# Kernel tuning notes

Measured on AMD Instinct MI355X. Metric: run time of the kernel, lower is better.

The kernel has to match this reference:

```python
import jax, jax.numpy as jnp
import numpy as np

TOPK_FRAC = 0.2

def _l2norm(v, eps=1e-12):
    return v / (jnp.linalg.norm(v) + eps)

def _spectral_normalize(w, u):
    # torch.nn.utils.spectral_norm forward: one power iteration (u,v detached),
    # sigma = u^T W v with gradient flowing through W only.
    wm = w.reshape(w.shape[0], -1)            # (out, in*kh*kw)
    v = _l2norm(jax.lax.stop_gradient(wm).T @ u)
    u_new = _l2norm(jax.lax.stop_gradient(wm) @ v)
    sigma = jnp.einsum('i,ij,j->', u_new, wm, v)
    return w / sigma

def setup_inputs() -> dict:
    key = jax.random.key(0)
    ks = jax.random.split(key, 5)
    N, C, H, W = 32, 512, 56, 56
    return {
        'x':  jax.random.normal(ks[0], (N, C, H, W), dtype=jnp.float32),
        'w1': jax.random.normal(ks[1], (C, C, 4, 4), dtype=jnp.float32) * 0.05,
        'w2': jax.random.normal(ks[2], (C, C, 1, 1), dtype=jnp.float32) * 0.05,
        'u1': jax.random.normal(ks[3], (C,), dtype=jnp.float32),
        'u2': jax.random.normal(ks[4], (C,), dtype=jnp.float32),
    }

def reference(x, w1, w2, u1, u2):
    N, C, H, W = x.shape
    # AdaptiveAvgPool2d(4): H,W divisible by 4 -> uniform 14x14 windows
    p = x.reshape(N, C, 4, H // 4, 4, W // 4).mean(axis=(3, 5))   # (N,C,4,4)
    p = jax.nn.sigmoid(p)
    # spectral-norm conv 4x4, valid, no bias -> fully reduces spatial to 1x1
    w1n = _spectral_normalize(w1, u1)                             # (C,C,4,4)
    h = jnp.einsum('ncij,ocij->no', p, w1n)                       # (N,C)
    h = jax.nn.relu(h)
    # spectral-norm conv 1x1
    w2n = _spectral_normalize(w2, u2).reshape(C, C)               # (out,in)
    s = jax.nn.sigmoid(jnp.einsum('nc,oc->no', h, w2n))           # (N,C)
    # sparse_ch: keep top int(0.2*C) channels per sample
    k = int(max(1, TOPK_FRAC * C))
    _, idx = jax.lax.top_k(s, k)                                  # (N,k)
    mask = jnp.zeros_like(s).at[jnp.arange(N)[:, None], idx].set(1.0)
    weight = (s * mask)[:, :, None, None]                         # (N,C,1,1)
    return x * weight
```

## Files before the change

kernel.cpp:

```cpp
#include <hip/hip_runtime.h>


#define KTOP 102

__device__ __forceinline__ float block_sum256(float v) {
  __shared__ float red[4];
  #pragma unroll
  for (int off = 32; off; off >>= 1) v += __shfl_down(v, off, 64);
  int lane = threadIdx.x & 63;
  int w = threadIdx.x >> 6;
  if (lane == 0) red[w] = v;
  __syncthreads();
  float r = 0.f;
  if (threadIdx.x == 0) r = red[0] + red[1] + red[2] + red[3];
  return r;
}

__global__ __launch_bounds__(256) void k_a(const float* __restrict__ x, const float* __restrict__ w1,
                                           const float* __restrict__ w2, const float* __restrict__ u1,
                                           const float* __restrict__ u2, float* __restrict__ p,
                                           float* __restrict__ part1, float* __restrict__ part1b,
                                           float* __restrict__ scal) {
  __shared__ float sx[3136];
  __shared__ float su[64];
  int b = blockIdx.x, t = threadIdx.x;
  if (b < 16384) {
    const float4* xp4 = (const float4*)(x + (size_t)b * 3136);
    float4* sx4 = (float4*)sx;
    for (int e = t; e < 784; e += 256) sx4[e] = xp4[e];
    __syncthreads();
    int w = t >> 4, lane = t & 15;
    int wr = w >> 2, wc = w & 3;
    float acc = 0.f;
    for (int e = lane; e < 196; e += 16) {
      int r = e / 14, cc = e - r * 14;
      acc += sx[(14 * wr + r) * 56 + 14 * wc + cc];
    }
    #pragma unroll
    for (int off = 8; off; off >>= 1) acc += __shfl_down(acc, off, 16);
    if (lane == 0) {
      float m = acc * (1.f / 196.f);
      p[(size_t)b * 16 + w] = 1.f / (1.f + expf(-m));
    }
  } else if (b < 16640) {
    int bb = b - 16384;
    if (bb == 0 && t < 4) scal[t] = 0.f;
    int jb = bb & 31, ic = bb >> 5;
    if (t < 64) su[t] = u1[ic * 64 + t];
    __syncthreads();
    int j = jb * 256 + t;
    const float* base = w1 + (size_t)(ic * 64) * 8192 + j;
    float acc = 0.f;
    #pragma unroll 4
    for (int i = 0; i < 64; ++i) acc += base[(size_t)i * 8192] * su[i];
    part1[ic * 8192 + j] = acc;
  } else {
    int bb = b - 16640;
    int jb = bb & 1, ic = bb >> 1;
    if (t < 64) su[t] = u2[ic * 64 + t];
    __syncthreads();
    int j = jb * 256 + t;
    const float* base = w2 + (size_t)(ic * 64) * 512 + j;
    float acc = 0.f;
    #pragma unroll 4
    for (int i = 0; i < 64; ++i) acc += base[(size_t)i * 512] * su[i];
    part1b[ic * 512 + j] = acc;
  }
}

__global__ __launch_bounds__(256) void k_b(const float* __restrict__ p, const float* __restrict__ w1,
                                           const float* __restrict__ part1, const float* __restrict__ part1b,
                                           float* __restrict__ part, float* __restrict__ t1,
                                           float* __restrict__ t1b, float* __restrict__ scal) {
  __shared__ float sp[32][132];
  __shared__ float sw[64][132];
  int b = blockIdx.x, t = threadIdx.x;
  if (b < 512) {
    int o0 = (b & 7) * 64;
    int k0 = (b >> 3) * 128;
    for (int idx = t; idx < 1024; idx += 256) {
      int r = idx >> 5, c4 = (idx & 31) << 2;
      *(float4*)&sp[r][c4] = *(const float4*)&p[(size_t)r * 8192 + k0 + c4];
    }
    for (int idx = t; idx < 2048; idx += 256) {
      int r = idx >> 5, c4 = (idx & 31) << 2;
      *(float4*)&sw[r][c4] = *(const float4*)&w1[(size_t)(o0 + r) * 8192 + k0 + c4];
    }
    __syncthreads();
    int m = t & 31, g = t >> 5;
    int n0 = g * 4;
    float acc[4][2] = {{0.f, 0.f}, {0.f, 0.f}, {0.f, 0.f}, {0.f, 0.f}};
    for (int kk = 0; kk < 128; kk += 4) {
      float4 wa = *(const float4*)&sw[m][kk];
      float4 wb = *(const float4*)&sw[m + 32][kk];
      #pragma unroll
      for (int ni = 0; ni < 4; ++ni) {
        float4 pv = *(const float4*)&sp[n0 + ni][kk];
        acc[ni][0] += pv.x * wa.x + pv.y * wa.y + pv.z * wa.z + pv.w * wa.w;
        acc[ni][1] += pv.x * wb.x + pv.y * wb.y + pv.z * wb.z + pv.w * wb.w;
      }
    }
    size_t base = (size_t)(b >> 3) * 16384;
    #pragma unroll
    for (int ni = 0; ni < 4; ++ni) {
      part[base + (n0 + ni) * 512 + o0 + m] = acc[ni][0];
      part[base + (n0 + ni) * 512 + o0 + m + 32] = acc[ni][1];
    }
  } else if (b < 544) {
    int j = (b - 512) * 256 + t;
    float s = 0.f;
    #pragma unroll
    for (int ic = 0; ic < 8; ++ic) s += part1[ic * 8192 + j];
    t1[j] = s;
    float tot = block_sum256(s * s);
    if (t == 0) atomicAdd(&scal[0], tot);
  } else {
    int j = (b - 544) * 256 + t;
    float s = 0.f;
    #pragma unroll
    for (int ic = 0; ic < 8; ++ic) s += part1b[ic * 512 + j];
    t1b[j] = s;
    float tot = block_sum256(s * s);
    if (t == 0) atomicAdd(&scal[1], tot);
  }
}

__global__ __launch_bounds__(256) void k_c(const float* __restrict__ part, const float* __restrict__ w1,
                                           const float* __restrict__ w2, const float* __restrict__ t1,
                                           const float* __restrict__ t1b, float* __restrict__ h,
                                           float* __restrict__ scal) {
  int b = blockIdx.x, t = threadIdx.x;
  if (b < 64) {
    int idx = b * 256 + t;
    float s = 0.f;
    for (int ks = 0; ks < 64; ++ks) s += part[(size_t)ks * 16384 + idx];
    h[idx] = fmaxf(s, 0.f);
  } else if (b < 576) {
    int i = b - 64;
    float inv = 1.f / (sqrtf(scal[0]) + 1e-12f);
    const float4* row = (const float4*)(w1 + (size_t)i * 8192);
    const float4* tv = (const float4*)t1;
    float acc = 0.f;
    for (int q = t; q < 2048; q += 256) {
      float4 a = row[q], v = tv[q];
      acc += a.x * v.x + a.y * v.y + a.z * v.z + a.w * v.w;
    }
    float tot = block_sum256(acc);
    if (t == 0) { float r = tot * inv; atomicAdd(&scal[2], r * r); }
  } else {
    int i = b - 576;
    float inv = 1.f / (sqrtf(scal[1]) + 1e-12f);
    const float4* row = (const float4*)(w2 + (size_t)i * 512);
    const float4* tv = (const float4*)t1b;
    float acc = 0.f;
    if (t < 128) {
      float4 a = row[t], v = tv[t];
      acc = a.x * v.x + a.y * v.y + a.z * v.z + a.w * v.w;
    }
    float tot = block_sum256(acc);
    if (t == 0) { float r = tot * inv; atomicAdd(&scal[3], r * r); }
  }
}

__global__ __launch_bounds__(256) void k_gemm2(const float* __restrict__ h, const float* __restrict__ w2,
                                               const float* __restrict__ scal, float* __restrict__ s_out) {
  int o = blockIdx.x, t = threadIdx.x;
  int w = t >> 6, lane = t & 63;
  float A2 = scal[2], B2 = scal[3];
  float sig1 = A2 / (sqrtf(A2) + 1e-12f);
  float sig2 = B2 / (sqrtf(B2) + 1e-12f);
  float inv = 1.f / (sig1 * sig2);
  const float4* wr = (const float4*)(w2 + (size_t)o * 512);
  float4 wa = wr[lane * 2], wb = wr[lane * 2 + 1];
  #pragma unroll
  for (int j = 0; j < 8; ++j) {
    int n = w * 8 + j;
    const float4* hr = (const float4*)(h + (size_t)n * 512);
    float4 ha = hr[lane * 2], hb = hr[lane * 2 + 1];
    float d = ha.x * wa.x + ha.y * wa.y + ha.z * wa.z + ha.w * wa.w
            + hb.x * wb.x + hb.y * wb.y + hb.z * wb.z + hb.w * wb.w;
    #pragma unroll
    for (int off = 32; off; off >>= 1) d += __shfl_down(d, off, 64);
    if (lane == 0) s_out[(size_t)n * 512 + o] = 1.f / (1.f + expf(-d * inv));
  }
}

__global__ __launch_bounds__(256) void k_topk(const float* __restrict__ s_in, float* __restrict__ wgt) {
  __shared__ float ss[512];
  __shared__ unsigned sb[512];
  __shared__ int cnt;
  int n = blockIdx.x, t = threadIdx.x;
  float v0 = s_in[(size_t)n * 512 + t];
  float v1 = s_in[(size_t)n * 512 + 256 + t];
  ss[t] = v0; ss[t + 256] = v1;
  sb[t] = __float_as_uint(v0); sb[t + 256] = __float_as_uint(v1);
  __syncthreads();
  int r = KTOP;
  unsigned prefix = 0u;
  for (int bit = 31; bit >= 0; --bit) {
    if (t == 0) cnt = 0;
    __syncthreads();
    unsigned hi = prefix | (1u << bit);
    unsigned mhi = ~((1u << bit) - 1u);
    unsigned long long c0 = __ballot((sb[t] & mhi) == hi);
    unsigned long long c1 = __ballot((sb[t + 256] & mhi) == hi);
    if ((t & 63) == 0) atomicAdd(&cnt, __popcll(c0) + __popcll(c1));
    __syncthreads();
    int c = cnt;
    __syncthreads();
    if (c >= r) prefix = hi; else r -= c;
  }
  if (t == 0) cnt = 0;
  __syncthreads();
  {
    unsigned long long g0 = __ballot(sb[t] > prefix);
    unsigned long long g1 = __ballot(sb[t + 256] > prefix);
    if ((t & 63) == 0) atomicAdd(&cnt, __popcll(g0) + __popcll(g1));
  }
  __syncthreads();
  int alloweq = KTOP - cnt;
  for (int e = t; e < 512; e += 256) {
    unsigned v = sb[e];
    bool keep = v > prefix;
    if (!keep && v == prefix) {
      int rank = 0;
      for (int j = 0; j < e; ++j) rank += (sb[j] == prefix);
      keep = rank < alloweq;
    }
    wgt[(size_t)n * 512 + e] = keep ? ss[e] : 0.f;
  }
}

__global__ __launch_bounds__(256) void k_scale(const float* __restrict__ x, const float* __restrict__ wgt,
                                               float* __restrict__ out) {
  int plane = blockIdx.x;
  float g = wgt[plane];
  const float4* xi = (const float4*)(x + (size_t)plane * 3136);
  float4* oo = (float4*)(out + (size_t)plane * 3136);
  for (int e = threadIdx.x; e < 784; e += 256) {
    float4 v = xi[e];
    v.x *= g; v.y *= g; v.z *= g; v.w *= g;
    oo[e] = v;
  }
}

extern "C" void kernel_launch(void* const* d_in, const int* in_sizes, int n_in,
                              void* d_out, int out_size, void* d_ws, size_t ws_size,
                              hipStream_t stream) {
  const float* x  = (const float*)d_in[0];
  const float* w1 = (const float*)d_in[1];
  const float* w2 = (const float*)d_in[2];
  const float* u1 = (const float*)d_in[3];
  const float* u2 = (const float*)d_in[4];
  float* out = (float*)d_out;
  float* ws = (float*)d_ws;

  float* scal   = ws + 0;
  float* t1     = ws + 4;
  float* t1b    = ws + 8196;
  float* p      = ws + 8708;
  float* part1  = ws + 270852;
  float* part1b = ws + 336388;
  float* part   = ws + 340484;
  float* h      = ws + 1389060;
  float* s      = ws + 1405444;
  float* wgt    = ws + 1421828;

  k_a<<<16656, 256, 0, stream>>>(x, w1, w2, u1, u2, p, part1, part1b, scal);
  k_b<<<546, 256, 0, stream>>>(p, w1, part1, part1b, part, t1, t1b, scal);
  k_c<<<1088, 256, 0, stream>>>(part, w1, w2, t1, t1b, h, scal);
  k_gemm2<<<512, 256, 0, stream>>>(h, w2, scal, s);
  k_topk<<<32, 256, 0, stream>>>(s, wgt);
  k_scale<<<16384, 256, 0, stream>>>(x, wgt, out);
}
```

Before: 457.6 us.

## Fuse h reduction, second GEMM and top-k into one kernel; persistent grids

```diff
diff --git a/kernel.cpp b/kernel.cpp
--- a/kernel.cpp
+++ b/kernel.cpp
@@ -24,26 +24,29 @@
   __shared__ float sx[3136];
   __shared__ float su[64];
   int b = blockIdx.x, t = threadIdx.x;
-  if (b < 16384) {
-    const float4* xp4 = (const float4*)(x + (size_t)b * 3136);
-    float4* sx4 = (float4*)sx;
-    for (int e = t; e < 784; e += 256) sx4[e] = xp4[e];
-    __syncthreads();
-    int w = t >> 4, lane = t & 15;
-    int wr = w >> 2, wc = w & 3;
-    float acc = 0.f;
-    for (int e = lane; e < 196; e += 16) {
-      int r = e / 14, cc = e - r * 14;
-      acc += sx[(14 * wr + r) * 56 + 14 * wc + cc];
-    }
-    #pragma unroll
-    for (int off = 8; off; off >>= 1) acc += __shfl_down(acc, off, 16);
-    if (lane == 0) {
-      float m = acc * (1.f / 196.f);
-      p[(size_t)b * 16 + w] = 1.f / (1.f + expf(-m));
-    }
-  } else if (b < 16640) {
-    int bb = b - 16384;
+  if (b < 2048) {
+    for (int plane = b; plane < 16384; plane += 2048) {
+      __syncthreads();
+      const float4* xp4 = (const float4*)(x + (size_t)plane * 3136);
+      float4* sx4 = (float4*)sx;
+      for (int e = t; e < 784; e += 256) sx4[e] = xp4[e];
+      __syncthreads();
+      int w = t >> 4, lane = t & 15;
+      int wr = w >> 2, wc = w & 3;
+      float acc = 0.f;
+      for (int e = lane; e < 196; e += 16) {
+        int r = e / 14, cc = e - r * 14;
+        acc += sx[(14 * wr + r) * 56 + 14 * wc + cc];
+      }
+      #pragma unroll
+      for (int off = 8; off; off >>= 1) acc += __shfl_down(acc, off, 16);
+      if (lane == 0) {
+        float m = acc * (1.f / 196.f);
+        p[(size_t)plane * 16 + w] = 1.f / (1.f + expf(-m));
+      }
+    }
+  } else if (b < 2304) {
+    int bb = b - 2048;
     if (bb == 0 && t < 4) scal[t] = 0.f;
     int jb = bb & 31, ic = bb >> 5;
     if (t < 64) su[t] = u1[ic * 64 + t];
@@ -55,7 +58,7 @@
     for (int i = 0; i < 64; ++i) acc += base[(size_t)i * 8192] * su[i];
     part1[ic * 8192 + j] = acc;
   } else {
-    int bb = b - 16640;
+    int bb = b - 2304;
     int jb = bb & 1, ic = bb >> 1;
     if (t < 64) su[t] = u2[ic * 64 + t];
     __syncthreads();
@@ -125,20 +128,13 @@
   }
 }
 
-__global__ __launch_bounds__(256) void k_c(const float* __restrict__ part, const float* __restrict__ w1,
-                                           const float* __restrict__ w2, const float* __restrict__ t1,
-                                           const float* __restrict__ t1b, float* __restrict__ h,
+__global__ __launch_bounds__(256) void k_c(const float* __restrict__ w1, const float* __restrict__ w2,
+                                           const float* __restrict__ t1, const float* __restrict__ t1b,
                                            float* __restrict__ scal) {
   int b = blockIdx.x, t = threadIdx.x;
-  if (b < 64) {
-    int idx = b * 256 + t;
-    float s = 0.f;
-    for (int ks = 0; ks < 64; ++ks) s += part[(size_t)ks * 16384 + idx];
-    h[idx] = fmaxf(s, 0.f);
-  } else if (b < 576) {
-    int i = b - 64;
+  if (b < 512) {
     float inv = 1.f / (sqrtf(scal[0]) + 1e-12f);
-    const float4* row = (const float4*)(w1 + (size_t)i * 8192);
+    const float4* row = (const float4*)(w1 + (size_t)b * 8192);
     const float4* tv = (const float4*)t1;
     float acc = 0.f;
     for (int q = t; q < 2048; q += 256) {
@@ -148,7 +144,7 @@
     float tot = block_sum256(acc);
     if (t == 0) { float r = tot * inv; atomicAdd(&scal[2], r * r); }
   } else {
-    int i = b - 576;
+    int i = b - 512;
     float inv = 1.f / (sqrtf(scal[1]) + 1e-12f);
     const float4* row = (const float4*)(w2 + (size_t)i * 512);
     const float4* tv = (const float4*)t1b;
@@ -162,40 +158,58 @@
   }
 }
 
-__global__ __launch_bounds__(256) void k_gemm2(const float* __restrict__ h, const float* __restrict__ w2,
-                                               const float* __restrict__ scal, float* __restrict__ s_out) {
-  int o = blockIdx.x, t = threadIdx.x;
-  int w = t >> 6, lane = t & 63;
+__global__ __launch_bounds__(256) void k_de(const float* __restrict__ part, const float* __restrict__ w2,
+                                            const float* __restrict__ scal, float* __restrict__ wgt) {
+  __shared__ float tile[64][516];
+  __shared__ float sh[512];
+  __shared__ float ss[512];
+  __shared__ unsigned sb[512];
+  __shared__ int cnt;
+  int n = blockIdx.x, t = threadIdx.x;
+  {
+    float a0 = 0.f, a1 = 0.f;
+    for (int ks = 0; ks < 64; ++ks) {
+      const float* pr = part + (size_t)ks * 16384 + (size_t)n * 512;
+      a0 += pr[t];
+      a1 += pr[t + 256];
+    }
+    sh[t] = fmaxf(a0, 0.f);
+    sh[t + 256] = fmaxf(a1, 0.f);
+  }
+  __syncthreads();
+  int g = t >> 2, r = t & 3;
+  float4 hreg[32];
+  #pragma unroll
+  for (int i = 0; i < 32; ++i) hreg[i] = *(const float4*)&sh[r * 128 + i * 4];
   float A2 = scal[2], B2 = scal[3];
   float sig1 = A2 / (sqrtf(A2) + 1e-12f);
   float sig2 = B2 / (sqrtf(B2) + 1e-12f);
   float inv = 1.f / (sig1 * sig2);
-  const float4* wr = (const float4*)(w2 + (size_t)o * 512);
-  float4 wa = wr[lane * 2], wb = wr[lane * 2 + 1];
-  #pragma unroll
-  for (int j = 0; j < 8; ++j) {
-    int n = w * 8 + j;
-    const float4* hr = (const float4*)(h + (size_t)n * 512);
-    float4 ha = hr[lane * 2], hb = hr[lane * 2 + 1];
-    float d = ha.x * wa.x + ha.y * wa.y + ha.z * wa.z + ha.w * wa.w
-            + hb.x * wb.x + hb.y * wb.y + hb.z * wb.z + hb.w * wb.w;
-    #pragma unroll
-    for (int off = 32; off; off >>= 1) d += __shfl_down(d, off, 64);
-    if (lane == 0) s_out[(size_t)n * 512 + o] = 1.f / (1.f + expf(-d * inv));
-  }
-}
-
-__global__ __launch_bounds__(256) void k_topk(const float* __restrict__ s_in, float* __restrict__ wgt) {
-  __shared__ float ss[512];
-  __shared__ unsigned sb[512];
-  __shared__ int cnt;
-  int n = blockIdx.x, t = threadIdx.x;
-  float v0 = s_in[(size_t)n * 512 + t];
-  float v1 = s_in[(size_t)n * 512 + 256 + t];
-  ss[t] = v0; ss[t + 256] = v1;
-  sb[t] = __float_as_uint(v0); sb[t + 256] = __float_as_uint(v1);
-  __syncthreads();
-  int r = KTOP;
+  for (int ti = 0; ti < 8; ++ti) {
+    int o0 = ti * 64;
+    __syncthreads();
+    for (int idx = t; idx < 8192; idx += 256) {
+      int row = idx >> 7, c4 = (idx & 127) << 2;
+      *(float4*)&tile[row][c4] = *(const float4*)&w2[(size_t)(o0 + row) * 512 + c4];
+    }
+    __syncthreads();
+    float d = 0.f;
+    #pragma unroll
+    for (int i = 0; i < 32; ++i) {
+      float4 wv = *(const float4*)&tile[g][r * 128 + i * 4];
+      float4 hv = hreg[i];
+      d += wv.x * hv.x + wv.y * hv.y + wv.z * hv.z + wv.w * hv.w;
+    }
+    d += __shfl_xor(d, 1, 64);
+    d += __shfl_xor(d, 2, 64);
+    if (r == 0) {
+      float sv = 1.f / (1.f + expf(-d * inv));
+      ss[o0 + g] = sv;
+      sb[o0 + g] = __float_as_uint(sv);
+    }
+  }
+  __syncthreads();
+  int rr = KTOP;
   unsigned prefix = 0u;
   for (int bit = 31; bit >= 0; --bit) {
     if (t == 0) cnt = 0;
@@ -208,7 +222,7 @@
     __syncthreads();
     int c = cnt;
     __syncthreads();
-    if (c >= r) prefix = hi; else r -= c;
+    if (c >= rr) prefix = hi; else rr -= c;
   }
   if (t == 0) cnt = 0;
   __syncthreads();
@@ -233,14 +247,15 @@
 
 __global__ __launch_bounds__(256) void k_scale(const float* __restrict__ x, const float* __restrict__ wgt,
                                                float* __restrict__ out) {
-  int plane = blockIdx.x;
-  float g = wgt[plane];
-  const float4* xi = (const float4*)(x + (size_t)plane * 3136);
-  float4* oo = (float4*)(out + (size_t)plane * 3136);
-  for (int e = threadIdx.x; e < 784; e += 256) {
-    float4 v = xi[e];
-    v.x *= g; v.y *= g; v.z *= g; v.w *= g;
-    oo[e] = v;
+  for (int plane = blockIdx.x; plane < 16384; plane += 2048) {
+    float g = wgt[plane];
+    const float4* xi = (const float4*)(x + (size_t)plane * 3136);
+    float4* oo = (float4*)(out + (size_t)plane * 3136);
+    for (int e = threadIdx.x; e < 784; e += 256) {
+      float4 v = xi[e];
+      v.x *= g; v.y *= g; v.z *= g; v.w *= g;
+      oo[e] = v;
+    }
   }
 }
 
@@ -262,14 +277,11 @@
   float* part1  = ws + 270852;
   float* part1b = ws + 336388;
   float* part   = ws + 340484;
-  float* h      = ws + 1389060;
-  float* s      = ws + 1405444;
-  float* wgt    = ws + 1421828;
-
-  k_a<<<16656, 256, 0, stream>>>(x, w1, w2, u1, u2, p, part1, part1b, scal);
+  float* wgt    = ws + 1389060;
+
+  k_a<<<2320, 256, 0, stream>>>(x, w1, w2, u1, u2, p, part1, part1b, scal);
   k_b<<<546, 256, 0, stream>>>(p, w1, part1, part1b, part, t1, t1b, scal);
-  k_c<<<1088, 256, 0, stream>>>(part, w1, w2, t1, t1b, h, scal);
-  k_gemm2<<<512, 256, 0, stream>>>(h, w2, scal, s);
-  k_topk<<<32, 256, 0, stream>>>(s, wgt);
-  k_scale<<<16384, 256, 0, stream>>>(x, wgt, out);
-}
+  k_c<<<1024, 256, 0, stream>>>(w1, w2, t1, t1b, scal);
+  k_de<<<32, 256, 0, stream>>>(part, w2, scal, wgt);
+  k_scale<<<2048, 256, 0, stream>>>(x, wgt, out);
+}
```

Result: slower. 529.5 us (+15.7%).
